# Kernel tuning notes

Hardware: AMD Instinct MI355X
Metric: run time of the kernel (lower is better)

The kernel has to match this reference:

```python
import jax, jax.numpy as jnp
import numpy as np

B, T, DMODEL, H, DK, DV, FF = 4, 1024, 1024, 16, 64, 64, 4096


def _weight_mask(dmodel, dk):
    # tril ones -> 0 on/below diag, -inf above (matches torch masked_fill)
    m = jnp.tril(jnp.ones((dmodel, dk), dtype=jnp.float32))
    return jnp.where(m == 0, -jnp.inf, 0.0).astype(jnp.float32)


def _mha(Q, K, V, Wq, Wk, Wv, Wo, maskout):
    dk = Wq.shape[-1]
    if maskout:
        mask = _weight_mask(Wq.shape[1], dk)[None]  # (1, dmodel, dk)
        # softmax over the dmodel axis of the masked weight tensors (axis -2)
        Wq = jax.nn.softmax(Wq + mask, axis=-2)
        Wk = jax.nn.softmax(Wk + mask, axis=-2)
    WqQ = jnp.einsum('btd,hdk->bhtk', Q, Wq)
    WkK = jnp.einsum('btd,hdk->bhtk', K, Wk)
    WvV = jnp.einsum('btd,hdv->bhtv', V, Wv)
    scores = jnp.einsum('bhtk,bhsk->bhts', WqQ, WkK) / jnp.sqrt(jnp.float32(dk))
    # NOTE: source softmaxes over axis -2 (the QUERY axis), not the key axis
    attn = jax.nn.softmax(scores, axis=-2)
    out = jnp.einsum('bhts,bhsv->bhtv', attn, WvV)
    b, h, t, dv = out.shape
    out = out.transpose(0, 2, 1, 3).reshape(b, t, h * dv)  # (B, T, dmodel)
    return out @ Wo


def _norm(x):
    mean = jnp.mean(x, axis=-1, keepdims=True)
    std = jnp.std(x, axis=-1, keepdims=True, ddof=1)  # torch.std is unbiased
    return (x - mean) / std


def setup_inputs() -> dict:
    key = jax.random.key(0)
    ks = jax.random.split(key, 14)
    s = 0.02
    return {
        'x': jax.random.normal(ks[0], (B, T, DMODEL), jnp.float32),
        'y': jax.random.normal(ks[1], (B, T, DMODEL), jnp.float32),
        'Wq1': jax.random.normal(ks[2], (H, DMODEL, DK), jnp.float32) * s,
        'Wk1': jax.random.normal(ks[3], (H, DMODEL, DK), jnp.float32) * s,
        'Wv1': jax.random.normal(ks[4], (H, DMODEL, DV), jnp.float32) * s,
        'Wo1': jax.random.normal(ks[5], (DMODEL, DMODEL), jnp.float32) * s,
        'Wq2': jax.random.normal(ks[6], (H, DMODEL, DK), jnp.float32) * s,
        'Wk2': jax.random.normal(ks[7], (H, DMODEL, DK), jnp.float32) * s,
        'Wv2': jax.random.normal(ks[8], (H, DMODEL, DV), jnp.float32) * s,
        'Wo2': jax.random.normal(ks[9], (DMODEL, DMODEL), jnp.float32) * s,
        'w_in': jax.random.normal(ks[10], (FF, DMODEL), jnp.float32) * s,
        'b_in': jax.random.normal(ks[11], (FF,), jnp.float32) * s,
        'w_out': jax.random.normal(ks[12], (DMODEL, FF), jnp.float32) * s,
        'b_out': jax.random.normal(ks[13], (DMODEL,), jnp.float32) * s,
    }


def reference(x, y, Wq1, Wk1, Wv1, Wo1, Wq2, Wk2, Wv2, Wo2, w_in, b_in, w_out, b_out):
    # masked self-attention on decoded seq y
    out1 = _norm(_mha(y, y, y, Wq1, Wk1, Wv1, Wo1, True) + y)
    # cross-attention against encoded seq x
    out2 = _norm(_mha(out1, x, x, Wq2, Wk2, Wv2, Wo2, False) + out1)
    ff = jax.nn.relu(out2 @ w_in.T + b_in) @ w_out.T + b_out
    out3 = _norm(ff + out2)
    return (x, out3)
```

## Files before the change

### kernel.cpp

```cpp
#include <hip/hip_runtime.h>
#include <hip/hip_bf16.h>

#define BB 4
#define TT 1024
#define DD 1024
#define HH 16
#define DKK 64
#define FFF 4096

typedef unsigned short u16;
typedef unsigned int u32;
typedef __attribute__((ext_vector_type(8))) short s16x8;
typedef __attribute__((ext_vector_type(4))) float f32x4;

static __device__ __forceinline__ float bf2f(u16 s) {
  union { u32 u; float f; } v; v.u = ((u32)s) << 16; return v.f;
}
static __device__ __forceinline__ u16 f2bf(float f) {
  union { float f; u32 u; } v; v.f = f;
  u32 r = v.u + 0x7FFFu + ((v.u >> 16) & 1u);
  return (u16)(r >> 16);
}

#define GLDS(gp, lp) __builtin_amdgcn_global_load_lds( \
    (const __attribute__((address_space(1))) u32*)(gp), \
    (__attribute__((address_space(3))) u32*)(lp), 16, 0, 0)

static __device__ __forceinline__ void swz_block(int& bx, int& by) {
  int gx = gridDim.x, gy = gridDim.y;
  int nwg = gx * gy;
  int orig = by * gx + bx;
  int q = nwg >> 3, r = nwg & 7;
  int xcd = orig & 7, sl = orig >> 3;
  int wgid = (xcd < r ? xcd * (q + 1) : r * (q + 1) + (xcd - r) * q) + sl;
  int g = gx << 3;
  int grp = wgid / g, rem = wgid % g;
  bx = rem >> 3;
  by = (grp << 3) + (rem & 7);
}

__global__ __launch_bounds__(256) void k_f2bf(const float* __restrict__ s, u16* __restrict__ d, int n) {
  int i = (blockIdx.x * 256 + threadIdx.x) * 4;
  if (i < n) {
    float4 v = *(const float4*)(s + i);
    u16 o[4] = { f2bf(v.x), f2bf(v.y), f2bf(v.z), f2bf(v.w) };
    *(ushort4*)(d + i) = *(ushort4*)o;
  }
}

__global__ __launch_bounds__(256) void k_combine_bf(const float* __restrict__ a, const float* __restrict__ b,
                                                    u16* __restrict__ d, int n) {
  int i = (blockIdx.x * 256 + threadIdx.x) * 4;
  if (i < n) {
    float4 va = *(const float4*)(a + i);
    float4 vb = *(const float4*)(b + i);
    u16 o[4] = { f2bf(va.x + vb.x), f2bf(va.y + vb.y), f2bf(va.z + vb.z), f2bf(va.w + vb.w) };
    *(ushort4*)(d + i) = *(ushort4*)o;
  }
}

__global__ __launch_bounds__(256) void k_xprep(const float* __restrict__ x, float* __restrict__ dout,
                                               u16* __restrict__ xb, int n) {
  int i = (blockIdx.x * 256 + threadIdx.x) * 4;
  if (i < n) {
    float4 v = *(const float4*)(x + i);
    *(float4*)(dout + i) = v;
    u16 o[4] = { f2bf(v.x), f2bf(v.y), f2bf(v.z), f2bf(v.w) };
    *(ushort4*)(xb + i) = *(ushort4*)o;
  }
}

__global__ __launch_bounds__(256) void k_softmax_w_bf(const float* __restrict__ W, u16* __restrict__ Bt) {
  int col = blockIdx.x;
  int h = col >> 6, k = col & 63;
  int tid = threadIdx.x;
  const float* w = W + ((size_t)h * DD) * DKK + k;
  __shared__ float red[256];
  float m = -1e30f;
  for (int d = k + tid; d < DD; d += 256) m = fmaxf(m, w[(size_t)d * DKK]);
  red[tid] = m; __syncthreads();
  for (int s = 128; s > 0; s >>= 1) { if (tid < s) red[tid] = fmaxf(red[tid], red[tid + s]); __syncthreads(); }
  m = red[0]; __syncthreads();
  float sum = 0.f;
  for (int d = k + tid; d < DD; d += 256) sum += __expf(w[(size_t)d * DKK] - m);
  red[tid] = sum; __syncthreads();
  for (int s = 128; s > 0; s >>= 1) { if (tid < s) red[tid] += red[tid + s]; __syncthreads(); }
  float inv = 1.f / red[0];
  for (int d = tid; d < DD; d += 256) {
    float v = (d >= k) ? __expf(w[(size_t)d * DKK] - m) * inv : 0.f;
    Bt[(size_t)col * DD + d] = f2bf(v);
  }
}

__global__ __launch_bounds__(256) void k_reorder_w_bf(const float* __restrict__ W, u16* __restrict__ Bt) {
  int d0 = blockIdx.x << 6, h = blockIdx.y;
  __shared__ float t[64][65];
  int tid = threadIdx.x;
  const float* src = W + (size_t)h * DD * DKK + (size_t)d0 * DKK;
  #pragma unroll
  for (int i = 0; i < 16; ++i) {
    int e = i * 256 + tid; int r = e >> 6, c = e & 63;
    t[r][c] = src[(size_t)r * DKK + c];
  }
  __syncthreads();
  #pragma unroll
  for (int i = 0; i < 16; ++i) {
    int e = i * 256 + tid; int c = e >> 6, r = e & 63;
    Bt[((size_t)(h * 64 + c)) * DD + d0 + r] = f2bf(t[r][c]);
  }
}

__global__ __launch_bounds__(256) void k_transpose_bf(const float* __restrict__ W, u16* __restrict__ Bt) {
  int k0 = blockIdx.x << 6, n0 = blockIdx.y << 6;
  __shared__ float t[64][65];
  int tid = threadIdx.x;
  #pragma unroll
  for (int i = 0; i < 16; ++i) {
    int e = i * 256 + tid; int r = e >> 6, c = e & 63;
    t[r][c] = W[(size_t)(k0 + r) * DD + n0 + c];
  }
  __syncthreads();
  #pragma unroll
  for (int i = 0; i < 16; ++i) {
    int e = i * 256 + tid; int c = e >> 6, r = e & 63;
    Bt[(size_t)(n0 + c) * DD + k0 + r] = f2bf(t[r][c]);
  }
}

__global__ __launch_bounds__(512) void k_mfma_nt(
    const u16* __restrict__ A, const u16* __restrict__ B,
    float* __restrict__ Cf, float* __restrict__ Cf2, float* __restrict__ Cf3, float* __restrict__ Cf4,
    u16* __restrict__ Cb, u16* __restrict__ Cb2, u16* __restrict__ Ct,
    const float* __restrict__ bias, int relu, int mode, int M, int N, int K) {
  __shared__ u16 SLDS[4 * 4096];
  int bx = blockIdx.x, by = blockIdx.y;
  swz_block(bx, by);
  int tid = threadIdx.x, wave = tid >> 6, lane = tid & 63;
  int row0 = by << 7, col0 = bx << 7;
  int wm = (wave >> 2) << 6;
  int wn = (wave & 3) << 5;

  int Ksl = K / gridDim.z;
  int kbase = blockIdx.z * Ksl;
  int kend = kbase + Ksl;

  f32x4 acc[4][2];
  #pragma unroll
  for (int m = 0; m < 4; ++m)
    #pragma unroll
    for (int n = 0; n < 2; ++n) acc[m][n] = f32x4{0.f, 0.f, 0.f, 0.f};

  int srow = tid >> 2, scol = (tid & 3) << 3;
  const u16* Ag = A + (size_t)(row0 + srow) * K + scol;
  const u16* Bg = B + (size_t)(col0 + srow) * K + scol;
  int wbase = wave << 9;

  int fr = lane & 15, kg = (lane >> 4) << 3;
  int ardo = (wm + fr) * 32 + kg;
  int brdo = 8192 + (wn + fr) * 32 + kg;

  auto STAGE = [&](int buf, int k0) {
    GLDS(Ag + k0, SLDS + buf * 4096 + wbase);
    GLDS(Bg + k0, SLDS + 8192 + buf * 4096 + wbase);
  };

  STAGE(0, kbase);
  __syncthreads();
  int cur = 0;
  for (int k0 = kbase; k0 < kend; k0 += 32) {
    int nxt = k0 + 32;
    if (nxt < kend) STAGE(cur ^ 1, nxt);
    const u16* Ard = SLDS + cur * 4096 + ardo;
    const u16* Brd = SLDS + cur * 4096 + brdo;
    s16x8 aF[4], bF[2];
    #pragma unroll
    for (int m = 0; m < 4; ++m) aF[m] = *(const s16x8*)(Ard + m * 16 * 32);
    #pragma unroll
    for (int n = 0; n < 2; ++n) bF[n] = *(const s16x8*)(Brd + n * 16 * 32);
    #pragma unroll
    for (int m = 0; m < 4; ++m)
      #pragma unroll
      for (int n = 0; n < 2; ++n)
        acc[m][n] = __builtin_amdgcn_mfma_f32_16x16x32_bf16(aF[m], bF[n], acc[m][n], 0, 0, 0);
    __syncthreads();
    cur ^= 1;
  }

  int fq = (lane >> 4) << 2;

  if (mode == 0 && (Cf || Cf2)) {
    int z = blockIdx.z;
    float* Cpart = (z == 0) ? Cf : ((z == 1) ? Cf2 : ((z == 2) ? Cf3 : Cf4));
    #pragma unroll
    for (int n = 0; n < 2; ++n) {
      int col = col0 + wn + n * 16 + fr;
      float bs = bias ? bias[col] : 0.f;
      #pragma unroll
      for (int m = 0; m < 4; ++m) {
        #pragma unroll
        for (int r = 0; r < 4; ++r) {
          float v = acc[m][n][r] + bs;
          if (relu) v = fmaxf(v, 0.f);
          Cpart[(size_t)(row0 + wm + m * 16 + fq + r) * N + col] = v;
        }
      }
    }
    return;
  }

  u16* dstRow = nullptr; u16* dstCol = nullptr;
  int rowPitch = 1024, colBase = col0 & 1023;
  if (mode == 0) { dstRow = Cb; rowPitch = N; colBase = col0; }
  else if (mode == 1) { int q = col0 >> 10; if (q == 0) dstRow = Cb; else if (q == 1) dstRow = Cb2; else dstCol = Ct; }
  else { int q = col0 >> 10; if (q == 0) dstRow = Cb; else dstCol = Ct; }

  u16* Ep = SLDS + wave * 2048;
  #pragma unroll
  for (int m = 0; m < 4; ++m) {
    #pragma unroll
    for (int n = 0; n < 2; ++n) {
      int col = col0 + wn + n * 16 + fr;
      float bs = bias ? bias[col] : 0.f;
      #pragma unroll
      for (int r = 0; r < 4; ++r) {
        float v = acc[m][n][r] + bs;
        if (relu) v = fmaxf(v, 0.f);
        Ep[(fq + r) * 40 + n * 16 + fr] = f2bf(v);
      }
    }
    if (dstRow) {
      int rw = lane >> 2, seg = lane & 3;
      const u16* src = Ep + rw * 40 + seg * 8;
      u16* gd = dstRow + (size_t)(row0 + wm + m * 16 + rw) * rowPitch + colBase + wn + seg * 8;
      *(uint4*)gd = *(const uint4*)src;
    } else {
      int c = lane >> 1, half = lane & 1;
      u16 tmp[8];
      #pragma unroll
      for (int j = 0; j < 8; ++j) tmp[j] = Ep[(half * 8 + j) * 40 + c];
      u16* gd = dstCol + (size_t)(colBase + wn + c) * 4096 + row0 + wm + m * 16 + half * 8;
      *(uint4*)gd = *(const uint4*)tmp;
    }
  }
}

static __device__ __forceinline__ void stage_tile512(const u16* __restrict__ g, int gp, u16* L, int tid) {
  int row = tid >> 3, col8 = (tid & 7) << 3;
  *(uint4*)(L + row * 72 + col8) = *(const uint4*)(g + (size_t)row * gp + col8);
}

__global__ __launch_bounds__(512) void k_attn_stats_mfma(const u16* __restrict__ Qb, const u16* __restrict__ Kb,
                                                         float* __restrict__ csum) {
  __shared__ u16 Ks[2 * 4608];
  __shared__ u16 Qs[4608];
  int tid = threadIdx.x, wave = tid >> 6, lane = tid & 63;
  int bh = blockIdx.x, b = bh >> 4, h = bh & 15;
  int s0 = blockIdx.y << 7;
  int tile = wave >> 2, sw = wave & 3;
  stage_tile512(Kb + ((size_t)(b * TT + s0)) * DD + h * 64, DD, Ks, tid);
  stage_tile512(Kb + ((size_t)(b * TT + s0 + 64)) * DD + h * 64, DD, Ks + 4608, tid);
  int row = tid >> 3, col8 = (tid & 7) << 3;
  const u16* Qg = Qb + ((size_t)(b * TT) + row) * DD + h * 64 + col8;
  uint4 qreg = *(const uint4*)Qg;
  __syncthreads();
  int fr = lane & 15, g = lane >> 4;
  const u16* Bbase = Ks + tile * 4608 + (sw * 16 + fr) * 72 + g * 8;
  const u16* Abase = Qs + fr * 72 + g * 8;
  s16x8 bF0 = *(const s16x8*)(Bbase);
  s16x8 bF1 = *(const s16x8*)(Bbase + 32);
  float sum = 0.f;
  for (int t0 = 0; t0 < TT; t0 += 64) {
    __syncthreads();
    *(uint4*)(Qs + row * 72 + col8) = qreg;
    __syncthreads();
    if (t0 + 64 < TT) qreg = *(const uint4*)(Qg + (size_t)(t0 + 64) * DD);
    #pragma unroll
    for (int mt = 0; mt < 4; ++mt) {
      f32x4 acc = f32x4{0.f, 0.f, 0.f, 0.f};
      s16x8 a0 = *(const s16x8*)(Abase + mt * 16 * 72);
      s16x8 a1 = *(const s16x8*)(Abase + mt * 16 * 72 + 32);
      acc = __builtin_amdgcn_mfma_f32_16x16x32_bf16(a0, bF0, acc, 0, 0, 0);
      acc = __builtin_amdgcn_mfma_f32_16x16x32_bf16(a1, bF1, acc, 0, 0, 0);
      sum += __expf(acc[0] * 0.125f) + __expf(acc[1] * 0.125f)
           + __expf(acc[2] * 0.125f) + __expf(acc[3] * 0.125f);
    }
  }
  sum += __shfl_xor(sum, 16, 64);
  sum += __shfl_xor(sum, 32, 64);
  if (lane < 16) csum[(size_t)bh * TT + s0 + tile * 64 + sw * 16 + lane] = sum;
}

__global__ __launch_bounds__(512) void k_attn_apply_mfma(const u16* __restrict__ Qb, const u16* __restrict__ Kb,
                                                         const u16* __restrict__ Vt,
                                                         const float* __restrict__ csum,
                                                         u16* __restrict__ Op) {
  __shared__ u16 Qs[2 * 4608];
  __shared__ u16 KV2[2 * 4608];
  __shared__ u16 Pl[8 * 1024];
  __shared__ float rcsL[64];
  u16* Ks = KV2;
  u16* VTs = KV2 + 4608;
  int tid = threadIdx.x, wave = tid >> 6, lane = tid & 63;
  int bh = blockIdx.x, b = bh >> 4, h = bh & 15;
  int t0 = blockIdx.y << 7;
  int tile = wave >> 2, tw = wave & 3;
  stage_tile512(Qb + ((size_t)(b * TT + t0)) * DD + h * 64, DD, Qs, tid);
  stage_tile512(Qb + ((size_t)(b * TT + t0 + 64)) * DD + h * 64, DD, Qs + 4608, tid);
  int row = tid >> 3, col8 = (tid & 7) << 3;
  const u16* Kg = Kb + ((size_t)(b * TT) + row) * DD + h * 64 + col8;
  const u16* Vg = Vt + ((size_t)(h * 64) + row) * 4096 + (size_t)b * TT + col8;
  const size_t cbase = (size_t)bh * TT;
  uint4 kreg = *(const uint4*)Kg;
  uint4 vreg = *(const uint4*)Vg;
  float rc0 = (tid < 64) ? csum[cbase + tid] : 0.f;
  __syncthreads();
  int fr = lane & 15, g = lane >> 4;
  const u16* QbF = Qs + tile * 4608 + (tw * 16 + fr) * 72 + g * 8;
  const u16* KaF = Ks + fr * 72 + g * 8;
  char* Pw = (char*)(Pl + wave * 1024);
  uint swz = ((uint)(lane & 7)) << 4;
  s16x8 qF0 = *(const s16x8*)(QbF);
  s16x8 qF1 = *(const s16x8*)(QbF + 32);
  f32x4 acc_o[4];
  #pragma unroll
  for (int nt = 0; nt < 4; ++nt) acc_o[nt] = f32x4{0.f, 0.f, 0.f, 0.f};

  for (int s0 = 0; s0 < TT; s0 += 64) {
    __syncthreads();
    *(uint4*)(Ks + row * 72 + col8) = kreg;
    *(uint4*)(VTs + row * 72 + col8) = vreg;
    if (tid < 64) rcsL[tid] = 1.f / rc0;
    __syncthreads();
    if (s0 + 64 < TT) {
      kreg = *(const uint4*)(Kg + (size_t)(s0 + 64) * DD);
      vreg = *(const uint4*)(Vg + s0 + 64);
      if (tid < 64) rc0 = csum[cbase + s0 + 64 + tid];
    }
    #pragma unroll
    for (int mt = 0; mt < 4; ++mt) {
      f32x4 acc = f32x4{0.f, 0.f, 0.f, 0.f};
      s16x8 a0 = *(const s16x8*)(KaF + mt * 16 * 72);
      s16x8 a1 = *(const s16x8*)(KaF + mt * 16 * 72 + 32);
      acc = __builtin_amdgcn_mfma_f32_16x16x32_bf16(a0, qF0, acc, 0, 0, 0);
      acc = __builtin_amdgcn_mfma_f32_16x16x32_bf16(a1, qF1, acc, 0, 0, 0);
      f32x4 rc4 = *(const f32x4*)&rcsL[mt * 16 + g * 4];
      u16 pb[4];
      #pragma unroll
      for (int r = 0; r < 4; ++r)
        pb[r] = f2bf(__expf(acc[r] * 0.125f) * rc4[r]);
      uint woff = (uint)fr * 128 + (uint)(mt * 16 + g * 4) * 2;
      uint2 wv; wv.x = (u32)pb[0] | ((u32)pb[1] << 16); wv.y = (u32)pb[2] | ((u32)pb[3] << 16);
      *(uint2*)(Pw + (woff ^ swz)) = wv;
    }
    uint rbase = (uint)fr * 128;
    s16x8 pF0 = *(const s16x8*)(Pw + ((rbase + g * 16) ^ swz));
    s16x8 pF1 = *(const s16x8*)(Pw + ((rbase + 64 + g * 16) ^ swz));
    #pragma unroll
    for (int nt = 0; nt < 4; ++nt) {
      s16x8 v0 = *(const s16x8*)(VTs + (nt * 16 + fr) * 72 + g * 8);
      s16x8 v1 = *(const s16x8*)(VTs + (nt * 16 + fr) * 72 + 32 + g * 8);
      acc_o[nt] = __builtin_amdgcn_mfma_f32_16x16x32_bf16(pF0, v0, acc_o[nt], 0, 0, 0);
      acc_o[nt] = __builtin_amdgcn_mfma_f32_16x16x32_bf16(pF1, v1, acc_o[nt], 0, 0, 0);
    }
  }
  __syncthreads();
  u16* Ep = KV2 + wave * 1088;
  #pragma unroll
  for (int nt = 0; nt < 4; ++nt)
    #pragma unroll
    for (int r = 0; r < 4; ++r)
      Ep[(g * 4 + r) * 68 + nt * 16 + fr] = f2bf(acc_o[nt][r]);
  {
    int rw = lane >> 2, seg = lane & 3;
    const u16* src = Ep + rw * 68 + seg * 16;
    u16* gd = Op + ((size_t)(b * TT + t0 + tile * 64 + tw * 16 + rw)) * DD + h * 64 + seg * 16;
    #pragma unroll
    for (int i = 0; i < 4; ++i) *(uint2*)(gd + i * 4) = *(const uint2*)(src + i * 4);
  }
}

__global__ __launch_bounds__(256) void k_add_norm(const float* __restrict__ A, const float* __restrict__ A2,
                                                  const float* __restrict__ A3, const float* __restrict__ A4,
                                                  const float* __restrict__ bias,
                                                  const float* __restrict__ Bv,
                                                  float* __restrict__ O, u16* __restrict__ Ob) {
  int row = blockIdx.x, tid = threadIdx.x;
  size_t base = (size_t)row * DD;
  __shared__ float red[256];
  float v[4]; float s = 0.f;
  #pragma unroll
  for (int i = 0; i < 4; ++i) {
    int c = tid + (i << 8);
    float t = A[base + c] + Bv[base + c];
    if (A2) t += A2[base + c];
    if (A3) t += A3[base + c];
    if (A4) t += A4[base + c];
    if (bias) t += bias[c];
    v[i] = t; s += t;
  }
  red[tid] = s; __syncthreads();
  for (int t = 128; t > 0; t >>= 1) { if (tid < t) red[tid] += red[tid + t]; __syncthreads(); }
  float mean = red[0] * (1.f / 1024.f);
  __syncthreads();
  float vs = 0.f;
  #pragma unroll
  for (int i = 0; i < 4; ++i) { float d = v[i] - mean; vs += d * d; }
  red[tid] = vs; __syncthreads();
  for (int t = 128; t > 0; t >>= 1) { if (tid < t) red[tid] += red[tid + t]; __syncthreads(); }
  float inv = rsqrtf(red[0] * (1.f / 1023.f));
  #pragma unroll
  for (int i = 0; i < 4; ++i) {
    float o = (v[i] - mean) * inv;
    O[base + tid + (i << 8)] = o;
    if (Ob) Ob[base + tid + (i << 8)] = f2bf(o);
  }
}

extern "C" void kernel_launch(void* const* d_in, const int* in_sizes, int n_in,
                              void* d_out, int out_size, void* d_ws, size_t ws_size,
                              hipStream_t stream) {
  (void)in_sizes; (void)n_in; (void)out_size; (void)ws_size;
  const float* x    = (const float*)d_in[0];
  const float* y    = (const float*)d_in[1];
  const float* Wq1  = (const float*)d_in[2];
  const float* Wk1  = (const float*)d_in[3];
  const float* Wv1  = (const float*)d_in[4];
  const float* Wo1  = (const float*)d_in[5];
  const float* Wq2  = (const float*)d_in[6];
  const float* Wk2  = (const float*)d_in[7];
  const float* Wv2  = (const float*)d_in[8];
  const float* Wo2  = (const float*)d_in[9];
  const float* w_in  = (const float*)d_in[10];
  const float* b_in  = (const float*)d_in[11];
  const float* w_out = (const float*)d_in[12];
  const float* b_out = (const float*)d_in[13];

  float* ws = (float*)d_ws;
  size_t off = 0;
  auto allocw = [&](size_t nw) { float* p = ws + off; off += nw; return p; };
  const size_t MR = (size_t)BB * TT;
  const size_t ND = MR * DD;

  u16* Bq   = (u16*)allocw(512 * 1024);
  u16* Bk   = (u16*)allocw(512 * 1024);
  u16* Bv   = (u16*)allocw(512 * 1024);
  u16* Bwo  = (u16*)allocw(512 * 1024);
  u16* Wi   = (u16*)allocw(2 * 1024 * 1024);
  u16* Wob  = (u16*)allocw(2 * 1024 * 1024);
  u16* xbf  = (u16*)allocw(ND / 2);
  u16* ybf  = (u16*)allocw(ND / 2);
  u16* REG  = (u16*)allocw(ND * 2);
  float* ff2  = allocw(ND);
  float* out1 = allocw(ND);
  float* out2 = allocw(ND);
  float* csum = allocw((size_t)BB * HH * TT);

  u16* Qb = REG;
  u16* Kb = REG + ND;
  u16* Vt = REG + 2 * ND;
  u16* Mb = REG + 3 * ND;
  u16* ff1b = REG;
  u16* out2bf = ybf;
  float* doutHi = (float*)d_out + ND;
  float* pXY = (float*)xbf;

  dim3 blk(256), blkG(512), blkA(512);
  dim3 gConv(4096);
  dim3 gSm(1024);
  dim3 gRw(16, 16);
  dim3 gQKV(24, 32);
  dim3 gKV(16, 32);
  dim3 gP2(8, 32, 2);
  dim3 gF1(32, 32);
  dim3 gFF2(8, 32, 4);
  dim3 gAttn(BB * HH, TT / 128);
  dim3 gNorm(MR);

  k_xprep<<<gConv, blk, 0, stream>>>(x, (float*)d_out, xbf, (int)ND);
  k_f2bf<<<gConv, blk, 0, stream>>>(y, ybf, (int)ND);
  k_f2bf<<<gConv, blk, 0, stream>>>(w_in, Wi, FFF * DD);
  k_f2bf<<<gConv, blk, 0, stream>>>(w_out, Wob, DD * FFF);

  k_softmax_w_bf<<<gSm, blk, 0, stream>>>(Wq1, Bq);
  k_softmax_w_bf<<<gSm, blk, 0, stream>>>(Wk1, Bk);
  k_reorder_w_bf<<<gRw, blk, 0, stream>>>(Wv1, Bv);
  k_transpose_bf<<<gRw, blk, 0, stream>>>(Wo1, Bwo);
  k_mfma_nt<<<gQKV, blkG, 0, stream>>>(ybf, Bq, nullptr, nullptr, nullptr, nullptr, Qb, Kb, Vt, nullptr, 0, 1, 4096, 3072, 1024);
  k_attn_stats_mfma<<<gAttn, blkA, 0, stream>>>(Qb, Kb, csum);
  k_attn_apply_mfma<<<gAttn, blkA, 0, stream>>>(Qb, Kb, Vt, csum, Mb);
  k_mfma_nt<<<gP2, blkG, 0, stream>>>(Mb, Bwo, ff2, out2, nullptr, nullptr, nullptr, nullptr, nullptr, nullptr, 0, 0, 4096, 1024, 1024);
  k_add_norm<<<gNorm, blk, 0, stream>>>(ff2, out2, nullptr, nullptr, nullptr, y, out1, Mb );

  k_reorder_w_bf<<<gRw, blk, 0, stream>>>(Wq2, Bq);
  k_reorder_w_bf<<<gRw, blk, 0, stream>>>(Wk2, Bk);
  k_reorder_w_bf<<<gRw, blk, 0, stream>>>(Wv2, Bv);
  k_transpose_bf<<<gRw, blk, 0, stream>>>(Wo2, Bwo);
  k_mfma_nt<<<gP2, blkG, 0, stream>>>(Mb , Bq, ff2, out2, nullptr, nullptr, nullptr, nullptr, nullptr, nullptr, 0, 0, 4096, 1024, 1024);
  k_combine_bf<<<gConv, blk, 0, stream>>>(ff2, out2, Qb, (int)ND);
  k_mfma_nt<<<gKV, blkG, 0, stream>>>(xbf, Bk, nullptr, nullptr, nullptr, nullptr, Kb, nullptr, Vt, nullptr, 0, 2, 4096, 2048, 1024);
  k_attn_stats_mfma<<<gAttn, blkA, 0, stream>>>(Qb, Kb, csum);
  k_attn_apply_mfma<<<gAttn, blkA, 0, stream>>>(Qb, Kb, Vt, csum, Mb);
  k_mfma_nt<<<gP2, blkG, 0, stream>>>(Mb, Bwo, ff2, doutHi, nullptr, nullptr, nullptr, nullptr, nullptr, nullptr, 0, 0, 4096, 1024, 1024);
  k_add_norm<<<gNorm, blk, 0, stream>>>(ff2, doutHi, nullptr, nullptr, nullptr, out1, out2, out2bf);

  k_mfma_nt<<<gF1, blkG, 0, stream>>>(out2bf, Wi, nullptr, nullptr, nullptr, nullptr, ff1b, nullptr, nullptr, b_in, 1, 0, 4096, 4096, 1024);
  k_mfma_nt<<<gFF2, blkG, 0, stream>>>(ff1b, Wob, ff2, doutHi, out1, pXY, nullptr, nullptr, nullptr, nullptr, 0, 0, 4096, 1024, 4096);
  k_add_norm<<<gNorm, blk, 0, stream>>>(ff2, doutHi, out1, pXY, b_out, out2, doutHi, nullptr);
}
```

Baseline: 433.5 us.

## Store split-K GEMM partials in bf16 and swizzle attention block order

Split-K GEMM partial results now go through the LDS-staged bf16 epilogue instead of being written as fp32 scatter stores, and the add-norm and combine kernels read the bf16 partials with vectorized loads. This halves partial-sum traffic and coalesces the stores, at the cost of rounding each partial to bf16 before reduction. Separately, the attention grid is remapped so that the tiles of one batch-head land on the same XCD, aiming at better L2 reuse of K/V. The add-norm kernel also moves to float4/ushort4 per-thread contiguous access.

```diff
diff --git a/kernel.cpp b/kernel.cpp
--- a/kernel.cpp
+++ b/kernel.cpp
@@ -39,6 +39,13 @@
   by = (grp << 3) + (rem & 7);
 }
 
+static __device__ __forceinline__ void swz_attn(int& tileIdx, int& bh) {
+  int orig = blockIdx.y * 8 + blockIdx.x;
+  int wgid = ((orig & 7) << 6) | (orig >> 3);
+  tileIdx = wgid & 7;
+  bh = wgid >> 3;
+}
+
 __global__ __launch_bounds__(256) void k_f2bf(const float* __restrict__ s, u16* __restrict__ d, int n) {
   int i = (blockIdx.x * 256 + threadIdx.x) * 4;
   if (i < n) {
@@ -48,13 +55,14 @@
   }
 }
 
-__global__ __launch_bounds__(256) void k_combine_bf(const float* __restrict__ a, const float* __restrict__ b,
+__global__ __launch_bounds__(256) void k_combine_bf(const u16* __restrict__ a, const u16* __restrict__ b,
                                                     u16* __restrict__ d, int n) {
   int i = (blockIdx.x * 256 + threadIdx.x) * 4;
   if (i < n) {
-    float4 va = *(const float4*)(a + i);
-    float4 vb = *(const float4*)(b + i);
-    u16 o[4] = { f2bf(va.x + vb.x), f2bf(va.y + vb.y), f2bf(va.z + vb.z), f2bf(va.w + vb.w) };
+    ushort4 va = *(const ushort4*)(a + i);
+    ushort4 vb = *(const ushort4*)(b + i);
+    u16 o[4] = { f2bf(bf2f(va.x) + bf2f(vb.x)), f2bf(bf2f(va.y) + bf2f(vb.y)),
+                 f2bf(bf2f(va.z) + bf2f(vb.z)), f2bf(bf2f(va.w) + bf2f(vb.w)) };
     *(ushort4*)(d + i) = *(ushort4*)o;
   }
 }
@@ -129,7 +137,7 @@
 
 __global__ __launch_bounds__(512) void k_mfma_nt(
     const u16* __restrict__ A, const u16* __restrict__ B,
-    float* __restrict__ Cf, float* __restrict__ Cf2, float* __restrict__ Cf3, float* __restrict__ Cf4,
+    u16* __restrict__ P0, u16* __restrict__ P1, u16* __restrict__ P2, u16* __restrict__ P3,
     u16* __restrict__ Cb, u16* __restrict__ Cb2, u16* __restrict__ Ct,
     const float* __restrict__ bias, int relu, int mode, int M, int N, int K) {
   __shared__ u16 SLDS[4 * 4096];
@@ -188,29 +196,15 @@
 
   int fq = (lane >> 4) << 2;
 
-  if (mode == 0 && (Cf || Cf2)) {
-    int z = blockIdx.z;
-    float* Cpart = (z == 0) ? Cf : ((z == 1) ? Cf2 : ((z == 2) ? Cf3 : Cf4));
-    #pragma unroll
-    for (int n = 0; n < 2; ++n) {
-      int col = col0 + wn + n * 16 + fr;
-      float bs = bias ? bias[col] : 0.f;
-      #pragma unroll
-      for (int m = 0; m < 4; ++m) {
-        #pragma unroll
-        for (int r = 0; r < 4; ++r) {
-          float v = acc[m][n][r] + bs;
-          if (relu) v = fmaxf(v, 0.f);
-          Cpart[(size_t)(row0 + wm + m * 16 + fq + r) * N + col] = v;
-        }
-      }
-    }
-    return;
-  }
-
   u16* dstRow = nullptr; u16* dstCol = nullptr;
   int rowPitch = 1024, colBase = col0 & 1023;
-  if (mode == 0) { dstRow = Cb; rowPitch = N; colBase = col0; }
+  if (mode == 0) {
+    rowPitch = N; colBase = col0;
+    if (gridDim.z > 1) {
+      int z = blockIdx.z;
+      dstRow = (z == 0) ? P0 : ((z == 1) ? P1 : ((z == 2) ? P2 : P3));
+    } else dstRow = Cb;
+  }
   else if (mode == 1) { int q = col0 >> 10; if (q == 0) dstRow = Cb; else if (q == 1) dstRow = Cb2; else dstCol = Ct; }
   else { int q = col0 >> 10; if (q == 0) dstRow = Cb; else dstCol = Ct; }
 
@@ -254,8 +248,10 @@
   __shared__ u16 Ks[2 * 4608];
   __shared__ u16 Qs[4608];
   int tid = threadIdx.x, wave = tid >> 6, lane = tid & 63;
-  int bh = blockIdx.x, b = bh >> 4, h = bh & 15;
-  int s0 = blockIdx.y << 7;
+  int tileIdx, bh;
+  swz_attn(tileIdx, bh);
+  int b = bh >> 4, h = bh & 15;
+  int s0 = tileIdx << 7;
   int tile = wave >> 2, sw = wave & 3;
   stage_tile512(Kb + ((size_t)(b * TT + s0)) * DD + h * 64, DD, Ks, tid);
   stage_tile512(Kb + ((size_t)(b * TT + s0 + 64)) * DD + h * 64, DD, Ks + 4608, tid);
@@ -301,8 +297,10 @@
   u16* Ks = KV2;
   u16* VTs = KV2 + 4608;
   int tid = threadIdx.x, wave = tid >> 6, lane = tid & 63;
-  int bh = blockIdx.x, b = bh >> 4, h = bh & 15;
-  int t0 = blockIdx.y << 7;
+  int tileIdx, bh;
+  swz_attn(tileIdx, bh);
+  int b = bh >> 4, h = bh & 15;
+  int t0 = tileIdx << 7;
   int tile = wave >> 2, tw = wave & 3;
   stage_tile512(Qb + ((size_t)(b * TT + t0)) * DD + h * 64, DD, Qs, tid);
   stage_tile512(Qb + ((size_t)(b * TT + t0 + 64)) * DD + h * 64, DD, Qs + 4608, tid);
@@ -379,25 +377,39 @@
   }
 }
 
-__global__ __launch_bounds__(256) void k_add_norm(const float* __restrict__ A, const float* __restrict__ A2,
-                                                  const float* __restrict__ A3, const float* __restrict__ A4,
+__global__ __launch_bounds__(256) void k_add_norm(const u16* __restrict__ A, const u16* __restrict__ A2,
+                                                  const u16* __restrict__ A3, const u16* __restrict__ A4,
                                                   const float* __restrict__ bias,
                                                   const float* __restrict__ Bv,
                                                   float* __restrict__ O, u16* __restrict__ Ob) {
   int row = blockIdx.x, tid = threadIdx.x;
   size_t base = (size_t)row * DD;
+  int c0 = tid * 4;
   __shared__ float red[256];
-  float v[4]; float s = 0.f;
-  #pragma unroll
-  for (int i = 0; i < 4; ++i) {
-    int c = tid + (i << 8);
-    float t = A[base + c] + Bv[base + c];
-    if (A2) t += A2[base + c];
-    if (A3) t += A3[base + c];
-    if (A4) t += A4[base + c];
-    if (bias) t += bias[c];
-    v[i] = t; s += t;
-  }
+  float v[4];
+  {
+    ushort4 a = *(const ushort4*)(A + base + c0);
+    float4 bv = *(const float4*)(Bv + base + c0);
+    v[0] = bf2f(a.x) + bv.x; v[1] = bf2f(a.y) + bv.y;
+    v[2] = bf2f(a.z) + bv.z; v[3] = bf2f(a.w) + bv.w;
+  }
+  if (A2) {
+    ushort4 a = *(const ushort4*)(A2 + base + c0);
+    v[0] += bf2f(a.x); v[1] += bf2f(a.y); v[2] += bf2f(a.z); v[3] += bf2f(a.w);
+  }
+  if (A3) {
+    ushort4 a = *(const ushort4*)(A3 + base + c0);
+    v[0] += bf2f(a.x); v[1] += bf2f(a.y); v[2] += bf2f(a.z); v[3] += bf2f(a.w);
+  }
+  if (A4) {
+    ushort4 a = *(const ushort4*)(A4 + base + c0);
+    v[0] += bf2f(a.x); v[1] += bf2f(a.y); v[2] += bf2f(a.z); v[3] += bf2f(a.w);
+  }
+  if (bias) {
+    float4 bs = *(const float4*)(bias + c0);
+    v[0] += bs.x; v[1] += bs.y; v[2] += bs.z; v[3] += bs.w;
+  }
+  float s = v[0] + v[1] + v[2] + v[3];
   red[tid] = s; __syncthreads();
   for (int t = 128; t > 0; t >>= 1) { if (tid < t) red[tid] += red[tid + t]; __syncthreads(); }
   float mean = red[0] * (1.f / 1024.f);
@@ -408,11 +420,13 @@
   red[tid] = vs; __syncthreads();
   for (int t = 128; t > 0; t >>= 1) { if (tid < t) red[tid] += red[tid + t]; __syncthreads(); }
   float inv = rsqrtf(red[0] * (1.f / 1023.f));
-  #pragma unroll
-  for (int i = 0; i < 4; ++i) {
-    float o = (v[i] - mean) * inv;
-    O[base + tid + (i << 8)] = o;
-    if (Ob) Ob[base + tid + (i << 8)] = f2bf(o);
+  float o[4];
+  #pragma unroll
+  for (int i = 0; i < 4; ++i) o[i] = (v[i] - mean) * inv;
+  *(float4*)(O + base + c0) = *(float4*)o;
+  if (Ob) {
+    u16 ob[4] = { f2bf(o[0]), f2bf(o[1]), f2bf(o[2]), f2bf(o[3]) };
+    *(ushort4*)(Ob + base + c0) = *(ushort4*)ob;
   }
 }
 
@@ -462,7 +476,10 @@
   u16* ff1b = REG;
   u16* out2bf = ybf;
   float* doutHi = (float*)d_out + ND;
-  float* pXY = (float*)xbf;
+  u16* p0 = (u16*)ff2;
+  u16* p1 = (u16*)ff2 + ND;
+  u16* p2 = (u16*)out1;
+  u16* p3 = (u16*)out1 + ND;
 
   dim3 blk(256), blkG(512), blkA(512);
   dim3 gConv(4096);
@@ -473,7 +490,7 @@
   dim3 gP2(8, 32, 2);
   dim3 gF1(32, 32);
   dim3 gFF2(8, 32, 4);
-  dim3 gAttn(BB * HH, TT / 128);
+  dim3 gAttn(8, 64);
   dim3 gNorm(MR);
 
   k_xprep<<<gConv, blk, 0, stream>>>(x, (float*)d_out, xbf, (int)ND);
@@ -488,22 +505,22 @@
   k_mfma_nt<<<gQKV, blkG, 0, stream>>>(ybf, Bq, nullptr, nullptr, nullptr, nullptr, Qb, Kb, Vt, nullptr, 0, 1, 4096, 3072, 1024);
   k_attn_stats_mfma<<<gAttn, blkA, 0, stream>>>(Qb, Kb, csum);
   k_attn_apply_mfma<<<gAttn, blkA, 0, stream>>>(Qb, Kb, Vt, csum, Mb);
-  k_mfma_nt<<<gP2, blkG, 0, stream>>>(Mb, Bwo, ff2, out2, nullptr, nullptr, nullptr, nullptr, nullptr, nullptr, 0, 0, 4096, 1024, 1024);
-  k_add_norm<<<gNorm, blk, 0, stream>>>(ff2, out2, nullptr, nullptr, nullptr, y, out1, Mb );
+  k_mfma_nt<<<gP2, blkG, 0, stream>>>(Mb, Bwo, p0, p1, nullptr, nullptr, nullptr, nullptr, nullptr, nullptr, 0, 0, 4096, 1024, 1024);
+  k_add_norm<<<gNorm, blk, 0, stream>>>(p0, p1, nullptr, nullptr, nullptr, y, out1, Mb );
 
   k_reorder_w_bf<<<gRw, blk, 0, stream>>>(Wq2, Bq);
   k_reorder_w_bf<<<gRw, blk, 0, stream>>>(Wk2, Bk);
   k_reorder_w_bf<<<gRw, blk, 0, stream>>>(Wv2, Bv);
   k_transpose_bf<<<gRw, blk, 0, stream>>>(Wo2, Bwo);
-  k_mfma_nt<<<gP2, blkG, 0, stream>>>(Mb , Bq, ff2, out2, nullptr, nullptr, nullptr, nullptr, nullptr, nullptr, 0, 0, 4096, 1024, 1024);
-  k_combine_bf<<<gConv, blk, 0, stream>>>(ff2, out2, Qb, (int)ND);
+  k_mfma_nt<<<gP2, blkG, 0, stream>>>(Mb , Bq, p0, p1, nullptr, nullptr, nullptr, nullptr, nullptr, nullptr, 0, 0, 4096, 1024, 1024);
+  k_combine_bf<<<gConv, blk, 0, stream>>>(p0, p1, Qb, (int)ND);
   k_mfma_nt<<<gKV, blkG, 0, stream>>>(xbf, Bk, nullptr, nullptr, nullptr, nullptr, Kb, nullptr, Vt, nullptr, 0, 2, 4096, 2048, 1024);
   k_attn_stats_mfma<<<gAttn, blkA, 0, stream>>>(Qb, Kb, csum);
   k_attn_apply_mfma<<<gAttn, blkA, 0, stream>>>(Qb, Kb, Vt, csum, Mb);
-  k_mfma_nt<<<gP2, blkG, 0, stream>>>(Mb, Bwo, ff2, doutHi, nullptr, nullptr, nullptr, nullptr, nullptr, nullptr, 0, 0, 4096, 1024, 1024);
-  k_add_norm<<<gNorm, blk, 0, stream>>>(ff2, doutHi, nullptr, nullptr, nullptr, out1, out2, out2bf);
+  k_mfma_nt<<<gP2, blkG, 0, stream>>>(Mb, Bwo, p0, p1, nullptr, nullptr, nullptr, nullptr, nullptr, nullptr, 0, 0, 4096, 1024, 1024);
+  k_add_norm<<<gNorm, blk, 0, stream>>>(p0, p1, nullptr, nullptr, nullptr, out1, out2, out2bf);
 
   k_mfma_nt<<<gF1, blkG, 0, stream>>>(out2bf, Wi, nullptr, nullptr, nullptr, nullptr, ff1b, nullptr, nullptr, b_in, 1, 0, 4096, 4096, 1024);
-  k_mfma_nt<<<gFF2, blkG, 0, stream>>>(ff1b, Wob, ff2, doutHi, out1, pXY, nullptr, nullptr, nullptr, nullptr, 0, 0, 4096, 1024, 4096);
-  k_add_norm<<<gNorm, blk, 0, stream>>>(ff2, doutHi, out1, pXY, b_out, out2, doutHi, nullptr);
-}
+  k_mfma_nt<<<gFF2, blkG, 0, stream>>>(ff1b, Wob, p0, p1, p2, p3, nullptr, nullptr, nullptr, nullptr, 0, 0, 4096, 1024, 4096);
+  k_add_norm<<<gNorm, blk, 0, stream>>>(p0, p1, p2, p3, b_out, out2, doutHi, nullptr);
+}
```

New measurement: 407.2 us. 6.1% less time.
